# Kernel optimization log

Hardware: AMD Instinct MI355X
Metric: run time of the kernel (lower is better)

Reference implementation:

```python
import jax, jax.numpy as jnp
import numpy as np

N_FLUID, N_BOX, K_MAX, KS, NCELL = 6000, 3000, 80, 4, 64
RADIUS = np.float32(0.5 * 1.5 * 6 * 0.025)  # filter_extent / 2 = 0.1125


def _ball_to_cube(p):
    """Volume-preserving ball->cube mapping (open3d ContinuousConv convention).
    p: [..., 3] coordinates in the unit ball; returns coords in [-1,1]^3."""
    eps = 1e-12
    x, y, z = p[..., 0], p[..., 1], p[..., 2]
    sq = x * x + y * y + z * z
    norm = jnp.sqrt(sq)
    rxy2 = x * x + y * y
    # sphere -> cylinder (volume preserving)
    polar = 1.25 * z * z > rxy2
    s_pol = jnp.sqrt(3.0 * norm / (norm + jnp.abs(z) + eps))
    s_eq = norm / jnp.sqrt(rxy2 + eps)
    xc = jnp.where(polar, s_pol * x, s_eq * x)
    yc = jnp.where(polar, s_pol * y, s_eq * y)
    zc = jnp.where(polar, jnp.sign(z) * norm, 1.5 * z * s_eq)
    zero = sq < 1e-12
    xc = jnp.where(zero, 0.0, xc)
    yc = jnp.where(zero, 0.0, yc)
    zc = jnp.where(zero, 0.0, zc)
    # cylinder -> cube (area-preserving disc -> square on xy)
    rxy = jnp.sqrt(xc * xc + yc * yc)
    FP = 4.0 / np.pi
    safe_x = jnp.where(jnp.abs(xc) < eps, eps, xc)
    safe_y = jnp.where(jnp.abs(yc) < eps, eps, yc)
    cond = jnp.abs(xc) >= jnp.abs(yc)
    u1 = jnp.sign(xc) * rxy
    v1 = u1 * FP * jnp.arctan(yc / safe_x)
    v2 = jnp.sign(yc) * rxy
    u2 = v2 * FP * jnp.arctan(xc / safe_y)
    u = jnp.where(cond, u1, u2)
    v = jnp.where(cond, v1, v2)
    small = rxy < eps
    u = jnp.where(small, 0.0, u)
    v = jnp.where(small, 0.0, v)
    return jnp.stack([u, v, zc], axis=-1)


def build_neighbors(pos_in, pos_out, ignore_self):
    """Fixed-radius neighbor search (capped at K_MAX) + window + trilinear
    interpolation cells/weights. Returns idx [No,K], cells [No,K,8] int32,
    coef [No,K,8] (trilinear weight * poly6 window * validity)."""
    d = pos_in[None, :, :] - pos_out[:, None, :]            # [No,Ni,3]
    d2 = jnp.sum(d * d, axis=-1)
    if ignore_self:
        ii = jnp.arange(pos_out.shape[0])
        d2 = jnp.where(ii[:, None] == ii[None, :], jnp.inf, d2)
    neg = jnp.where(d2 <= RADIUS * RADIUS, -d2, -jnp.inf)
    vals, idx = jax.lax.top_k(neg, K_MAX)                   # [No,K]
    valid = (vals > -jnp.inf).astype(pos_in.dtype)
    rel = (pos_in[idx] - pos_out[:, None, :]) / RADIUS      # [No,K,3] unit ball
    r2 = jnp.sum(rel * rel, axis=-1)
    win = jnp.clip((1.0 - r2) ** 3, 0.0, 1.0) * valid       # poly6 window
    g = jnp.clip((_ball_to_cube(rel) + 1.0) * 0.5 * (KS - 1), 0.0, KS - 1.0)
    i0 = jnp.clip(jnp.floor(g), 0, KS - 2).astype(jnp.int32)
    t = g - i0.astype(g.dtype)
    cells, tw = [], []
    for dx in (0, 1):
        for dy in (0, 1):
            for dz in (0, 1):
                w = ((t[..., 0] if dx else 1.0 - t[..., 0])
                     * (t[..., 1] if dy else 1.0 - t[..., 1])
                     * (t[..., 2] if dz else 1.0 - t[..., 2]))
                cell = ((i0[..., 2] + dz) * KS + (i0[..., 1] + dy)) * KS + (i0[..., 0] + dx)
                cells.append(cell)
                tw.append(w)
    cells = jnp.stack(cells, axis=-1)                       # [No,K,8]
    coef = jnp.stack(tw, axis=-1) * win[..., None]          # [No,K,8]
    return idx, cells, coef


def apply_cconv(feats_in, idx, cells, coef, W, b):
    """Continuous conv: scatter neighbor feats into 64 kernel cells per query,
    then contract with the filter. W: [64, F, O]."""
    N, K = idx.shape
    F = feats_in.shape[-1]
    nf = feats_in[idx]                                      # [N,K,F]
    S = jnp.zeros((N * NCELL, F), feats_in.dtype)
    row = (jnp.arange(N, dtype=jnp.int32) * NCELL)[:, None]
    for c in range(8):                                      # 8 trilinear corners
        flat = (row + cells[..., c]).reshape(-1)
        S = S.at[flat].add((coef[..., c:c + 1] * nf).reshape(-1, F))
    return jnp.einsum('ncf,cfo->no', S.reshape(N, NCELL, F), W) + b


def setup_inputs() -> dict:
    key = jax.random.key(0)
    ks = jax.random.split(key, 16)

    def p(i, shape, scale=0.05):
        return (scale * jax.random.normal(ks[i], shape)).astype(jnp.float32)

    return {
        'pos': jax.random.uniform(ks[0], (N_FLUID, 3), dtype=jnp.float32),
        'vel': jax.random.normal(ks[1], (N_FLUID, 3), dtype=jnp.float32),
        'box': jax.random.uniform(ks[2], (N_BOX, 3), dtype=jnp.float32),
        'box_feats': jax.random.normal(ks[3], (N_BOX, 3), dtype=jnp.float32),
        'cf_w': p(4, (NCELL, 4, 32)), 'cf_b': jnp.zeros((32,), jnp.float32),
        'co_w': p(5, (NCELL, 3, 32)), 'co_b': jnp.zeros((32,), jnp.float32),
        'd0_w': p(6, (4, 32)), 'd0_b': jnp.zeros((32,), jnp.float32),
        'c1_w': p(7, (NCELL, 96, 64)), 'c1_b': jnp.zeros((64,), jnp.float32),
        'd1_w': p(8, (96, 64)), 'd1_b': jnp.zeros((64,), jnp.float32),
        'c2_w': p(9, (NCELL, 64, 64)), 'c2_b': jnp.zeros((64,), jnp.float32),
        'd2_w': p(10, (64, 64)), 'd2_b': jnp.zeros((64,), jnp.float32),
        'c3_w': p(11, (NCELL, 64, 3)), 'c3_b': jnp.zeros((3,), jnp.float32),
        'd3_w': p(12, (64, 3)), 'd3_b': jnp.zeros((3,), jnp.float32),
    }


def reference(pos, vel, box, box_feats, cf_w, cf_b, co_w, co_b, d0_w, d0_b,
              c1_w, c1_b, d1_w, d1_b, c2_w, c2_b, d2_w, d2_b, c3_w, c3_b,
              d3_w, d3_b):
    fidx, fcells, fcoef = build_neighbors(pos, pos, True)
    oidx, ocells, ocoef = build_neighbors(box, pos, False)
    ff = jnp.concatenate([jnp.ones_like(pos[:, :1]), vel], axis=-1)  # [N,4]
    a_cf = apply_cconv(ff, fidx, fcells, fcoef, cf_w, cf_b)
    a_co = apply_cconv(box_feats, oidx, ocells, ocoef, co_w, co_b)
    a_d0 = ff @ d0_w + d0_b
    x = jnp.concatenate([a_co, a_cf, a_d0], axis=-1)                 # [N,96]
    for cw, cb, dw, db in ((c1_w, c1_b, d1_w, d1_b),
                           (c2_w, c2_b, d2_w, d2_b),
                           (c3_w, c3_b, d3_w, d3_b)):
        h = jax.nn.relu(x)
        y = apply_cconv(h, fidx, fcells, fcoef, cw, cb) + (h @ dw + db)
        x = y + x if y.shape[-1] == x.shape[-1] else y
    return x * (1.0 / 128.0)  # pos_correction [N,3]
```

## Files before the change

### kernel.cpp

```cpp
#include <hip/hip_runtime.h>
#include <math.h>

namespace {

constexpr int NQ  = 6000;
constexpr int NB  = 3000;
constexpr int K   = 80;
constexpr float RAD = 0.1125f;
constexpr float R2  = RAD * RAD;
constexpr float EPSF = 1e-12f;

constexpr int GS  = 8;
constexpr int NC  = GS*GS*GS;
constexpr int NO  = 65 * 64;
constexpr int NBLK = (NQ + 3) / 4;
constexpr int NBLK8 = ((NBLK + 7) / 8) * 8;

typedef __attribute__((ext_vector_type(8))) short bf16x8;
typedef __attribute__((ext_vector_type(4))) float f32x4;

__device__ __forceinline__ float sgn(float x) {
    return (x > 0.f) ? 1.f : ((x < 0.f) ? -1.f : 0.f);
}

__device__ __forceinline__ unsigned int bf16rne(float f) {
    unsigned int u = __float_as_uint(f);
    return (u + 0x7fffu + ((u >> 16) & 1u)) >> 16;
}
__device__ __forceinline__ float bf16f(unsigned short u) {
    return __uint_as_float(((unsigned int)u) << 16);
}
__device__ __forceinline__ int cell_of(float x, float y, float z) {
    int cx = min(max((int)(x * (float)GS), 0), GS-1);
    int cy = min(max((int)(y * (float)GS), 0), GS-1);
    int cz = min(max((int)(z * (float)GS), 0), GS-1);
    return (cz*GS + cy)*GS + cx;
}

__device__ void coef_store(float ddx, float ddy, float ddz, int slot,
                           int* __restrict__ cells, float* __restrict__ coefs)
{
    float rx = ddx / RAD, ry = ddy / RAD, rz = ddz / RAD;
    float r2 = rx*rx + ry*ry + rz*rz;
    float w1 = 1.f - r2;
    float win = (w1 > 0.f) ? w1*w1*w1 : 0.f;
    float norm = sqrtf(r2);
    float rxy2 = rx*rx + ry*ry;
    float xc, yc, zc;
    if (r2 < 1e-12f) {
        xc = yc = zc = 0.f;
    } else if (1.25f * rz * rz > rxy2) {
        float s = sqrtf(3.0f * norm / (norm + fabsf(rz) + EPSF));
        xc = s * rx; yc = s * ry; zc = sgn(rz) * norm;
    } else {
        float s = norm / sqrtf(rxy2 + EPSF);
        xc = s * rx; yc = s * ry; zc = 1.5f * rz * s;
    }
    float rxy = sqrtf(xc*xc + yc*yc);
    const float FP = (float)(4.0 / M_PI);
    float u, v;
    if (rxy < EPSF) {
        u = 0.f; v = 0.f;
    } else if (fabsf(xc) >= fabsf(yc)) {
        float sx = (fabsf(xc) < EPSF) ? EPSF : xc;
        u = sgn(xc) * rxy;
        v = u * FP * atanf(yc / sx);
    } else {
        float sy = (fabsf(yc) < EPSF) ? EPSF : yc;
        v = sgn(yc) * rxy;
        u = v * FP * atanf(xc / sy);
    }
    float gx = fminf(fmaxf((u  + 1.f) * 0.5f * 3.f, 0.f), 3.f);
    float gy = fminf(fmaxf((v  + 1.f) * 0.5f * 3.f, 0.f), 3.f);
    float gz = fminf(fmaxf((zc + 1.f) * 0.5f * 3.f, 0.f), 3.f);
    int ix = min((int)floorf(gx), 2);
    int iy = min((int)floorf(gy), 2);
    int iz = min((int)floorf(gz), 2);
    float tx = gx - (float)ix, ty = gy - (float)iy, tz = gz - (float)iz;
    cells[slot] = iz*16 + iy*4 + ix;
    float wx[2] = {1.f - tx, tx}, wy[2] = {1.f - ty, ty}, wz[2] = {1.f - tz, tz};
    float* cf = coefs + (size_t)slot * 8;
#pragma unroll
    for (int c = 0; c < 8; ++c)
        cf[c] = wx[c >> 2] * wy[(c >> 1) & 1] * wz[c & 1] * win;
}

__global__ __launch_bounds__(512) void scan_kernel(
    const int* __restrict__ gcnt,
    int* __restrict__ gs_f, int* __restrict__ gs_b,
    int* __restrict__ cur_f, int* __restrict__ cur_b)
{
    __shared__ int tmp[NC];
    int tid = threadIdx.x;
#pragma unroll
    for (int a = 0; a < 2; ++a) {
        int cntv = gcnt[a*NC + tid];
        tmp[tid] = cntv;
        __syncthreads();
        for (int off = 1; off < NC; off <<= 1) {
            int v = (tid >= off) ? tmp[tid - off] : 0;
            __syncthreads();
            tmp[tid] += v;
            __syncthreads();
        }
        int* gsd = a ? gs_b : gs_f;
        int* cur = a ? cur_b : cur_f;
        int excl = tmp[tid] - cntv;
        gsd[tid] = excl;
        cur[tid] = excl;
        if (tid == NC - 1) gsd[NC] = tmp[tid];
        __syncthreads();
    }
}

__global__ __launch_bounds__(256) void scatter_pts_kernel(
    const float* __restrict__ pos, const float* __restrict__ box,
    int* __restrict__ cur_f, int* __restrict__ cur_b,
    float* __restrict__ spf, int* __restrict__ sif,
    float* __restrict__ spb, int* __restrict__ sib)
{
    int t = blockIdx.x * blockDim.x + threadIdx.x;
    if (t < NQ) {
        float x = pos[t*3], y = pos[t*3+1], z = pos[t*3+2];
        int dst = atomicAdd(&cur_f[cell_of(x,y,z)], 1);
        spf[dst*3] = x; spf[dst*3+1] = y; spf[dst*3+2] = z;
        sif[dst] = t;
    } else if (t < NQ + NB) {
        int b = t - NQ;
        float x = box[b*3], y = box[b*3+1], z = box[b*3+2];
        int dst = atomicAdd(&cur_b[cell_of(x,y,z)], 1);
        spb[dst*3] = x; spb[dst*3+1] = y; spb[dst*3+2] = z;
        sib[dst] = b;
    }
}

__global__ __launch_bounds__(256) void nn2gc_kernel(
    const float* __restrict__ pos,
    const float* __restrict__ spf, const int* __restrict__ sif, const int* __restrict__ gsf,
    const float* __restrict__ spb, const int* __restrict__ sib, const int* __restrict__ gsb,
    int* __restrict__ f_cnt, int* __restrict__ f_idx, float* __restrict__ f_d2,
    int* __restrict__ f_cell, float* __restrict__ f_coef,
    int* __restrict__ b_cnt, int* __restrict__ b_idx, float* __restrict__ b_d2,
    int* __restrict__ b_cell, float* __restrict__ b_coef)
{
    int gw = (blockIdx.x * blockDim.x + threadIdx.x) >> 6;
    int lane = threadIdx.x & 63;
    if (gw >= 2 * NQ) return;
    bool isF = gw < NQ;
    int wid = isF ? gw : gw - NQ;
    const float* sp = isF ? spf : spb;
    const int*   si = isF ? sif : sib;
    const int*   gs = isF ? gsf : gsb;
    int*   cnt   = isF ? f_cnt  : b_cnt;
    int*   idxs  = isF ? f_idx  : b_idx;
    float* d2s   = isF ? f_d2   : b_d2;
    int*   cells = isF ? f_cell : b_cell;
    float* coefs = isF ? f_coef : b_coef;
    float qx = pos[wid*3+0], qy = pos[wid*3+1], qz = pos[wid*3+2];
    int cx = min(max((int)(qx * (float)GS), 0), GS-1);
    int cy = min(max((int)(qy * (float)GS), 0), GS-1);
    int cz = min(max((int)(qz * (float)GS), 0), GS-1);
    int x0 = max(cx-1, 0), x1 = min(cx+1, GS-1);
    int base = wid * K;
    int c = 0;
    for (int dz = -1; dz <= 1; ++dz) {
        int z = cz + dz; if ((unsigned)z >= (unsigned)GS) continue;
        for (int dy = -1; dy <= 1; ++dy) {
            int y = cy + dy; if ((unsigned)y >= (unsigned)GS) continue;
            int row = (z*GS + y)*GS;
            int s0 = gs[row + x0], s1 = gs[row + x1 + 1];
            for (int j0 = s0; j0 < s1; j0 += 64) {
                int ii = j0 + lane;
                float d2 = 1e30f; int oj = 0;
                float ddx = 0.f, ddy = 0.f, ddz = 0.f;
                if (ii < s1) {
                    oj = si[ii];
                    ddx = sp[ii*3+0]-qx; ddy = sp[ii*3+1]-qy; ddz = sp[ii*3+2]-qz;
                    d2 = ddx*ddx + ddy*ddy + ddz*ddz;
                    if (isF && oj == wid) d2 = 1e30f;
                }
                bool hit = d2 <= R2;
                unsigned long long m = __ballot(hit);
                int pc = __popcll(m);
                if (pc == 0) continue;
                if (c + pc <= K) {
                    if (hit) {
                        int p = c + __popcll(m & ((1ull << lane) - 1ull));
                        idxs[base + p] = oj;
                        d2s [base + p] = d2;
                        coef_store(ddx, ddy, ddz, base + p, cells, coefs);
                    }
                    c += pc;
                } else {
                    while (m) {
                        int l = __ffsll((unsigned long long)m) - 1;
                        m &= m - 1ull;
                        float dd = __shfl(d2, l);
                        int jv = __shfl(oj, l);
                        float ax = __shfl(ddx, l), ay = __shfl(ddy, l), az = __shfl(ddz, l);
                        int slot = -1;
                        if (c < K) { slot = c; c++; }
                        else {
                            float mx = -1.f; int am = 0;
                            for (int s = 0; s < K; ++s) {
                                float v = d2s[base + s];
                                if (v > mx) { mx = v; am = s; }
                            }
                            if (dd < mx) slot = am;
                        }
                        if (slot >= 0 && lane == 0) {
                            idxs[base + slot] = jv;
                            d2s [base + slot] = dd;
                            coef_store(ax, ay, az, base + slot, cells, coefs);
                        }
                    }
                }
            }
        }
    }
    if (lane == 0) cnt[wid] = c;
}

template<int F>
__device__ void scatter_small_dev(
    const float* __restrict__ feats,
    const int* __restrict__ cnt, const int* __restrict__ nidx,
    const int* __restrict__ ncell, const float* __restrict__ ncoef,
    float* __restrict__ Sg, int blk)
{
    __shared__ __align__(16) float S4[4][64 * F];
    int tid = threadIdx.x, lane = tid & 63, w = tid >> 6;
    int n = blk * 4 + w;
    if (n >= NQ) return;
    float* Sw = S4[w];
    for (int i = lane; i < 64 * F; i += 64) Sw[i] = 0.f;
    int cn = cnt[n];
    int kk2 = 64 + lane;
    int cb1 = (lane < cn) ? ncell[n*K + lane] : 0;
    int j1  = (lane < cn) ? nidx [n*K + lane] : 0;
    int cb2 = (kk2 < cn) ? ncell[n*K + kk2] : 0;
    int j2  = (kk2 < cn) ? nidx [n*K + kk2] : 0;
    int c = lane & 7, f = lane >> 3;
    bool fok = f < F;
    const float* coefG = ncoef + (size_t)n * K * 8;

    float wgt = 0.f, v = 0.f; int cb = 0;
    if (cn > 0) {
        int j = __shfl(j1, 0); cb = __shfl(cb1, 0);
        if (fok) { wgt = coefG[c]; v = feats[(size_t)j * F + f]; }
    }
    for (int kk = 0; kk < cn; ++kk) {
        float wn = 0.f, vn = 0.f; int cbn = 0;
        int k1n = kk + 1;
        if (k1n < cn) {
            int jn = (k1n < 64) ? __shfl(j1, k1n) : __shfl(j2, k1n - 64);
            cbn    = (k1n < 64) ? __shfl(cb1, k1n) : __shfl(cb2, k1n - 64);
            if (fok) { wn = coefG[k1n*8 + c]; vn = feats[(size_t)jn * F + f]; }
        }
        if (fok) {
            int cell = cb + (c & 1)*16 + ((c >> 1) & 1)*4 + (c >> 2);
            Sw[cell*F + f] += wgt * v;
        }
        wgt = wn; v = vn; cb = cbn;
    }
    float* row = Sg + (size_t)n * (64 * F);
    for (int i = lane; i < 16 * F; i += 64)
        ((float4*)row)[i] = ((const float4*)Sw)[i];
}

__global__ __launch_bounds__(256) void scatter0_kernel(
    const float* __restrict__ ff,
    const int* __restrict__ f_cnt, const int* __restrict__ f_idx,
    const int* __restrict__ f_cell, const float* __restrict__ f_coef,
    const float* __restrict__ bfeat,
    const int* __restrict__ b_cnt, const int* __restrict__ b_idx,
    const int* __restrict__ b_cell, const float* __restrict__ b_coef,
    float* __restrict__ S_cf, float* __restrict__ S_co)
{
    constexpr int FB = (NQ + 3) / 4;
    if (blockIdx.x < FB)
        scatter_small_dev<4>(ff, f_cnt, f_idx, f_cell, f_coef, S_cf, blockIdx.x);
    else
        scatter_small_dev<3>(bfeat, b_cnt, b_idx, b_cell, b_coef, S_co, blockIdx.x - FB);
}

__global__ __launch_bounds__(256) void gemm0_kernel(
    const float* __restrict__ S_co, const float* __restrict__ S_cf,
    const float* __restrict__ coW, const float* __restrict__ cfW,
    const float* __restrict__ cob, const float* __restrict__ cfb,
    float* __restrict__ x1, int M)
{
    constexpr int O = 32, TX = 8, MT = 128, ASTR = 132;
    __shared__ float As[16][ASTR];
    __shared__ float Bs[16 * O];
    int which = blockIdx.y;
    const float* A    = which ? S_cf : S_co;
    const float* B    = which ? cfW  : coW;
    const float* bias = which ? cfb  : cob;
    int Kdim = which ? 256 : 192;
    int ooff = which ? 32 : 0;
    int tid = threadIdx.x;
    int tx = tid % TX, ty = tid / TX;
    int m0 = blockIdx.x * MT;
    int ntiles = Kdim >> 4;
    float acc[4][4] = {};
    for (int t = 0; t < ntiles; ++t) {
        int k0 = t << 4;
        __syncthreads();
#pragma unroll
        for (int l = 0; l < 2; ++l) {
            int idx = tid + l * 256;
            int mm = idx >> 2, k4 = idx & 3;
            int gm = m0 + mm; if (gm >= M) gm = M - 1;
            float4 av = *reinterpret_cast<const float4*>(A + (size_t)gm * Kdim + k0 + k4 * 4);
            As[k4*4+0][mm] = av.x; As[k4*4+1][mm] = av.y;
            As[k4*4+2][mm] = av.z; As[k4*4+3][mm] = av.w;
        }
        if (tid < 128)
            *reinterpret_cast<float4*>(&Bs[tid*4]) =
                *reinterpret_cast<const float4*>(B + (size_t)k0 * O + tid * 4);
        __syncthreads();
#pragma unroll
        for (int kk = 0; kk < 16; ++kk) {
            float4 av = *reinterpret_cast<const float4*>(&As[kk][ty*4]);
            float4 bv = *reinterpret_cast<const float4*>(&Bs[kk*O + tx*4]);
            float aa[4] = {av.x, av.y, av.z, av.w};
            float bb[4] = {bv.x, bv.y, bv.z, bv.w};
#pragma unroll
            for (int i = 0; i < 4; ++i)
#pragma unroll
                for (int jj = 0; jj < 4; ++jj)
                    acc[i][jj] += aa[i] * bb[jj];
        }
    }
#pragma unroll
    for (int i = 0; i < 4; ++i) {
        int gm = m0 + ty*4 + i;
        if (gm < M)
#pragma unroll
            for (int jj = 0; jj < 4; ++jj)
                x1[(size_t)gm * 96 + ooff + tx*4 + jj] = acc[i][jj] + bias[tx*4 + jj];
    }
}

template<int F>
__global__ __launch_bounds__(256) void gemmGm_kernel(
    const float* __restrict__ feats,
    const unsigned short* __restrict__ Bt,
    unsigned short* __restrict__ G,
    int M)
{
    constexpr int AST = F + 8;
    __shared__ unsigned short As[64 * AST];
    __shared__ unsigned short Bs[64 * AST];
    int tid = threadIdx.x, lane = tid & 63, wv = tid >> 6;
    int m0 = blockIdx.x * 64, no0 = blockIdx.y * 64;
    for (int i = tid; i < 64 * F / 4; i += 256) {
        int m = i / (F / 4), k4 = i % (F / 4);
        int gm = m0 + m; if (gm >= M) gm = M - 1;
        float4 av = *reinterpret_cast<const float4*>(feats + (size_t)gm * F + k4 * 4);
        uint2 o;
        o.x = bf16rne(fmaxf(av.x, 0.f)) | (bf16rne(fmaxf(av.y, 0.f)) << 16);
        o.y = bf16rne(fmaxf(av.z, 0.f)) | (bf16rne(fmaxf(av.w, 0.f)) << 16);
        *reinterpret_cast<uint2*>(As + m * AST + k4 * 4) = o;
    }
    for (int i = tid; i < 64 * F / 8; i += 256) {
        int n = i / (F / 8), k8 = i % (F / 8);
        *reinterpret_cast<uint4*>(Bs + n * AST + k8 * 8) =
            *reinterpret_cast<const uint4*>(Bt + (size_t)(no0 + n) * F + k8 * 8);
    }
    __syncthreads();
    int mr = lane & 15, quad = lane >> 4;
    f32x4 acc[4] = {{0.f,0.f,0.f,0.f},{0.f,0.f,0.f,0.f},
                    {0.f,0.f,0.f,0.f},{0.f,0.f,0.f,0.f}};
#pragma unroll
    for (int kc = 0; kc < F; kc += 32) {
        bf16x8 a = *reinterpret_cast<const bf16x8*>(As + (wv*16 + mr) * AST + kc + quad*8);
#pragma unroll
        for (int t = 0; t < 4; ++t) {
            bf16x8 b = *reinterpret_cast<const bf16x8*>(Bs + (t*16 + mr) * AST + kc + quad*8);
            acc[t] = __builtin_amdgcn_mfma_f32_16x16x32_bf16(a, b, acc[t], 0, 0, 0);
        }
    }
#pragma unroll
    for (int t = 0; t < 4; ++t) {
#pragma unroll
        for (int r = 0; r < 4; ++r) {
            int gm = m0 + wv*16 + quad*4 + r;
            if (gm < M)
                G[(size_t)gm * NO + no0 + t*16 + mr] = (unsigned short)bf16rne(acc[t][r]);
        }
    }
}

template<int FUSEY>
__global__ __launch_bounds__(256) void gatherG_kernel(
    const int* __restrict__ order,
    const int* __restrict__ cnt, const int* __restrict__ nidx,
    const int* __restrict__ ncell, const float* __restrict__ ncoef,
    const unsigned short* __restrict__ G,
    const float* __restrict__ cb, const float* __restrict__ db,
    const float* __restrict__ resid, float* __restrict__ out,
    const float* __restrict__ W3p, float* __restrict__ Y)
{
    __shared__ __align__(16) float coefL[K * 8];
    __shared__ int jL[K];
    __shared__ int cbL[K];
    __shared__ float part[3][64];
    __shared__ float xs[64];
    int lb = (blockIdx.x & 7) * (gridDim.x >> 3) + (blockIdx.x >> 3);
    int tid = threadIdx.x;
    int wv = tid >> 6, lane = tid & 63;
    int n = order[lb];
    int cn = cnt[n];
    {
        const float4* src = (const float4*)(ncoef + (size_t)n * K * 8);
        float4* dst = (float4*)coefL;
        for (int i = tid; i < cn * 2; i += 256) dst[i] = src[i];
        for (int i = tid; i < cn; i += 256) {
            jL[i]  = nidx [n*K + i];
            cbL[i] = ncell[n*K + i];
        }
    }
    __syncthreads();
    float a0 = 0.f, a1 = 0.f, a2 = 0.f, a3 = 0.f;
#pragma unroll 2
    for (int k = wv; k < cn; k += 4) {
        int j    = jL[k];
        int cbse = cbL[k];
        float4 cA = *reinterpret_cast<const float4*>(coefL + k*8);
        float4 cB = *reinterpret_cast<const float4*>(coefL + k*8 + 4);
        const unsigned short* Gj = G + (size_t)j * NO + (size_t)cbse * 64 + lane;
        a0 += cA.x * bf16f(Gj[ 0 * 64]);
        a1 += cA.y * bf16f(Gj[16 * 64]);
        a2 += cA.z * bf16f(Gj[ 4 * 64]);
        a3 += cA.w * bf16f(Gj[20 * 64]);
        a0 += cB.x * bf16f(Gj[ 1 * 64]);
        a1 += cB.y * bf16f(Gj[17 * 64]);
        a2 += cB.z * bf16f(Gj[ 5 * 64]);
        a3 += cB.w * bf16f(Gj[21 * 64]);
    }
    float s = (a0 + a1) + (a2 + a3);
    if (wv > 0) part[wv - 1][lane] = s;
    __syncthreads();
    if (wv == 0) {
        float acc = cb[lane] + db[lane] + s
                  + part[0][lane] + part[1][lane] + part[2][lane];
        acc += bf16f(G[(size_t)n * NO + 64*64 + lane]);
        if (resid) acc += resid[(size_t)n * 64 + lane];
        if (!FUSEY) {
            out[(size_t)n * 64 + lane] = acc;
        } else {
            xs[lane] = fmaxf(acc, 0.f);
        }
    }
    if (FUSEY) {
        __syncthreads();
        for (int t = tid; t < 195; t += 256) {
            float sum = 0.f;
#pragma unroll 16
            for (int f = 0; f < 64; ++f) sum += xs[f] * W3p[f*195 + t];
            Y[(size_t)n * 195 + t] = sum;
        }
    }
}

__global__ __launch_bounds__(256) void prep_kernel(
    const float* __restrict__ c1w, const float* __restrict__ d1w,
    const float* __restrict__ c2w, const float* __restrict__ d2w,
    const float* __restrict__ c3w, const float* __restrict__ d3w,
    const float* __restrict__ pos, const float* __restrict__ box,
    const float* __restrict__ vel,
    const float* __restrict__ d0w, const float* __restrict__ d0b,
    unsigned short* __restrict__ Bt1, unsigned short* __restrict__ Bt2,
    float* __restrict__ W3p, float* __restrict__ ff, float* __restrict__ x1,
    int* __restrict__ gcnt)
{
    int stride = gridDim.x * blockDim.x;
    int gid = blockIdx.x * blockDim.x + threadIdx.x;
    for (int i = gid; i < NQ + NB; i += stride) {
        const float* p = (i < NQ) ? pos + (size_t)i*3 : box + (size_t)(i-NQ)*3;
        atomicAdd(&gcnt[((i < NQ) ? 0 : NC) + cell_of(p[0], p[1], p[2])], 1);
    }
    for (int i = gid; i < NO * 96; i += stride) {
        int n = i / 96, f = i % 96, c = n >> 6, o = n & 63;
        float v = (c < 64) ? c1w[((size_t)c*96 + f)*64 + o] : d1w[f*64 + o];
        Bt1[i] = (unsigned short)bf16rne(v);
    }
    for (int i = gid; i < NO * 64; i += stride) {
        int n = i / 64, f = i % 64, c = n >> 6, o = n & 63;
        float v = (c < 64) ? c2w[((size_t)c*64 + f)*64 + o] : d2w[f*64 + o];
        Bt2[i] = (unsigned short)bf16rne(v);
    }
    for (int i = gid; i < 64 * 195; i += stride) {
        int f = i / 195, r = i % 195, c = r / 3, o = r % 3;
        W3p[i] = (c < 64) ? c3w[(c*64 + f)*3 + o] : d3w[f*3 + o];
    }
    for (int i = gid; i < NQ; i += stride) {
        ff[i*4+0] = 1.f;
        ff[i*4+1] = vel[i*3+0];
        ff[i*4+2] = vel[i*3+1];
        ff[i*4+3] = vel[i*3+2];
    }
    for (int i = gid; i < NQ * 32; i += stride) {
        int n = i >> 5, o = i & 31;
        float acc = d0b[o] + d0w[o]
                  + vel[n*3+0] * d0w[32 + o]
                  + vel[n*3+1] * d0w[64 + o]
                  + vel[n*3+2] * d0w[96 + o];
        x1[n*96 + 64 + o] = acc;
    }
}

__global__ __launch_bounds__(256) void gather3_kernel(
    const int* __restrict__ order,
    const int* __restrict__ cnt, const int* __restrict__ nidx,
    const int* __restrict__ ncell, const float* __restrict__ ncoef,
    const float* __restrict__ Y,
    const float* __restrict__ cb3, const float* __restrict__ db3,
    float* __restrict__ out)
{
    int lb = (blockIdx.x & 7) * (gridDim.x >> 3) + (blockIdx.x >> 3);
    int gw = lb * 4 + ((int)threadIdx.x >> 6);
    int lane = threadIdx.x & 63;
    if (gw >= NQ) return;
    int n = order[gw];
    int cn = cnt[n];
    float a0 = 0.f, a1 = 0.f, a2 = 0.f;
#pragma unroll
    for (int seg = 0; seg < 2; ++seg) {
        int kidx = seg * 64 + lane;
        if (kidx < cn) {
            int j  = nidx [n*K + kidx];
            int cb = ncell[n*K + kidx];
            const float* cf = ncoef + (size_t)(n*K + kidx) * 8;
            const float* Yj = Y + (size_t)j * 195;
#pragma unroll
            for (int c = 0; c < 8; ++c) {
                int cell = cb + (c & 1)*16 + ((c >> 1) & 1)*4 + (c >> 2);
                float wgt = cf[c];
                const float* Tp = Yj + cell*3;
                a0 += wgt * Tp[0];
                a1 += wgt * Tp[1];
                a2 += wgt * Tp[2];
            }
        }
    }
#pragma unroll
    for (int s = 32; s > 0; s >>= 1) {
        a0 += __shfl_down(a0, s);
        a1 += __shfl_down(a1, s);
        a2 += __shfl_down(a2, s);
    }
    if (lane == 0) {
        const float* Yn = Y + (size_t)n * 195 + 192;
        out[n*3+0] = (a0 + Yn[0] + cb3[0] + db3[0]) * (1.f/128.f);
        out[n*3+1] = (a1 + Yn[1] + cb3[1] + db3[1]) * (1.f/128.f);
        out[n*3+2] = (a2 + Yn[2] + cb3[2] + db3[2]) * (1.f/128.f);
    }
}

}

extern "C" void kernel_launch(void* const* d_in, const int* in_sizes, int n_in,
                              void* d_out, int out_size, void* d_ws, size_t ws_size,
                              hipStream_t stream)
{
    const float* pos       = (const float*)d_in[0];
    const float* vel       = (const float*)d_in[1];
    const float* box       = (const float*)d_in[2];
    const float* box_feats = (const float*)d_in[3];
    const float* cf_w = (const float*)d_in[4];  const float* cf_b = (const float*)d_in[5];
    const float* co_w = (const float*)d_in[6];  const float* co_b = (const float*)d_in[7];
    const float* d0_w = (const float*)d_in[8];  const float* d0_b = (const float*)d_in[9];
    const float* c1_w = (const float*)d_in[10]; const float* c1_b = (const float*)d_in[11];
    const float* d1_w = (const float*)d_in[12]; const float* d1_b = (const float*)d_in[13];
    const float* c2_w = (const float*)d_in[14]; const float* c2_b = (const float*)d_in[15];
    const float* d2_w = (const float*)d_in[16]; const float* d2_b = (const float*)d_in[17];
    const float* c3_w = (const float*)d_in[18]; const float* c3_b = (const float*)d_in[19];
    const float* d3_w = (const float*)d_in[20]; const float* d3_b = (const float*)d_in[21];

    char* wsb = (char*)d_ws;
    size_t off = 0;
    auto alloc = [&](size_t bytes) {
        void* p = wsb + off;
        off = (off + bytes + 255) & ~(size_t)255;
        return p;
    };
    char*  Graw = (char*)alloc((size_t)NQ * NO * 2 + 4096);
    unsigned short* G = (unsigned short*)Graw;
    float* f_d2 = (float*)Graw;
    float* b_d2 = (float*)Graw + (size_t)NQ * K;
    float* S_cf = (float*)Graw;
    float* S_co = (float*)Graw + (size_t)NQ * 256;
    int*   f_cnt  = (int*)  alloc((size_t)NQ * 4);
    int*   f_idx  = (int*)  alloc((size_t)NQ * K * 4);
    int*   f_cell = (int*)  alloc((size_t)NQ * K * 4);
    float* f_coef = (float*)alloc((size_t)NQ * K * 8 * 4);
    int*   b_cnt  = (int*)  alloc((size_t)NQ * 4);
    int*   b_idx  = (int*)  alloc((size_t)NQ * K * 4);
    int*   b_cell = (int*)  alloc((size_t)NQ * K * 4);
    float* b_coef = (float*)alloc((size_t)NQ * K * 8 * 4);
    float* ff     = (float*)alloc((size_t)NQ * 4 * 4);
    float* x1     = (float*)alloc((size_t)NQ * 96 * 4);
    float* x2     = (float*)alloc((size_t)NQ * 64 * 4);
    unsigned short* Bt1 = (unsigned short*)alloc((size_t)NO * 96 * 2);
    unsigned short* Bt2 = (unsigned short*)alloc((size_t)NO * 64 * 2);
    float* W3p    = (float*)alloc((size_t)64 * 195 * 4);
    float* Y      = (float*)alloc((size_t)NQ * 195 * 4);
    int*   gcnt   = (int*)  alloc((size_t)2 * NC * 4);
    int*   gs_f   = (int*)  alloc((size_t)(NC + 1) * 4);
    int*   gs_b   = (int*)  alloc((size_t)(NC + 1) * 4);
    int*   cur_f  = (int*)  alloc((size_t)NC * 4);
    int*   cur_b  = (int*)  alloc((size_t)NC * 4);
    float* spf    = (float*)alloc((size_t)NQ * 3 * 4);
    int*   sif    = (int*)  alloc((size_t)NQ * 4);
    float* spb    = (float*)alloc((size_t)NB * 3 * 4);
    int*   sib    = (int*)  alloc((size_t)NB * 4);

    dim3 b256(256);
    hipMemsetAsync(gcnt, 0, (size_t)2 * NC * 4, stream);
    prep_kernel<<<512, b256, 0, stream>>>(c1_w, d1_w, c2_w, d2_w, c3_w, d3_w,
                                          pos, box, vel, d0_w, d0_b,
                                          Bt1, Bt2, W3p, ff, x1, gcnt);
    scan_kernel<<<1, 512, 0, stream>>>(gcnt, gs_f, gs_b, cur_f, cur_b);
    scatter_pts_kernel<<<(NQ + NB + 255)/256, b256, 0, stream>>>(
        pos, box, cur_f, cur_b, spf, sif, spb, sib);
    nn2gc_kernel<<<(2*NQ*64 + 255)/256, b256, 0, stream>>>(
        pos, spf, sif, gs_f, spb, sib, gs_b,
        f_cnt, f_idx, f_d2, f_cell, f_coef,
        b_cnt, b_idx, b_d2, b_cell, b_coef);
    scatter0_kernel<<<2*((NQ+3)/4), b256, 0, stream>>>(
        ff, f_cnt, f_idx, f_cell, f_coef,
        box_feats, b_cnt, b_idx, b_cell, b_coef, S_cf, S_co);
    gemm0_kernel<<<dim3((NQ+127)/128, 2), b256, 0, stream>>>(
        S_co, S_cf, co_w, cf_w, co_b, cf_b, x1, NQ);
    gemmGm_kernel<96><<<dim3((NQ+63)/64, NO/64), b256, 0, stream>>>(x1, Bt1, G, NQ);
    gatherG_kernel<0><<<NQ, b256, 0, stream>>>(sif, f_cnt, f_idx, f_cell, f_coef,
        G, c1_b, d1_b, nullptr, x2, nullptr, nullptr);
    gemmGm_kernel<64><<<dim3((NQ+63)/64, NO/64), b256, 0, stream>>>(x2, Bt2, G, NQ);
    gatherG_kernel<1><<<NQ, b256, 0, stream>>>(sif, f_cnt, f_idx, f_cell, f_coef,
        G, c2_b, d2_b, x2, nullptr, W3p, Y);
    gather3_kernel<<<NBLK8, b256, 0, stream>>>(sif, f_cnt, f_idx, f_cell, f_coef,
        Y, c3_b, d3_b, (float*)d_out);

    (void)in_sizes; (void)n_in; (void)out_size; (void)ws_size;
    (void)f_d2; (void)b_d2;
}
```

Before: 281.9 us.

## Precompute per-point cell projections for first conv layer and gather instead of scatter+GEMM

Replaces the first-layer scatter into per-point cell buffers followed by an FP32 GEMM with a precomputed per-source-point table (features times per-cell weights, stored as bf16) built in the prep kernel. A new gather kernel then sums trilinear-weighted table entries over neighbours. This drops the scatter-to-LDS pass and the separate gemm0 launch, at the cost of writing two large bf16 tables in prep and reduced precision. Separately, the MFMA G-GEMM now loops over 5 output tiles per block, keeping the A tile resident and shrinking the grid y-dimension from 65 to 13.

Measured after the change: 270.0 us. -4.2%, faster.

```diff
diff --git a/kernel.cpp b/kernel.cpp
--- a/kernel.cpp
+++ b/kernel.cpp
@@ -221,125 +221,82 @@
     if (lane == 0) cnt[wid] = c;
 }
 
-template<int F>
-__device__ void scatter_small_dev(
-    const float* __restrict__ feats,
-    const int* __restrict__ cnt, const int* __restrict__ nidx,
-    const int* __restrict__ ncell, const float* __restrict__ ncoef,
-    float* __restrict__ Sg, int blk)
-{
-    __shared__ __align__(16) float S4[4][64 * F];
-    int tid = threadIdx.x, lane = tid & 63, w = tid >> 6;
-    int n = blk * 4 + w;
-    if (n >= NQ) return;
-    float* Sw = S4[w];
-    for (int i = lane; i < 64 * F; i += 64) Sw[i] = 0.f;
-    int cn = cnt[n];
-    int kk2 = 64 + lane;
-    int cb1 = (lane < cn) ? ncell[n*K + lane] : 0;
-    int j1  = (lane < cn) ? nidx [n*K + lane] : 0;
-    int cb2 = (kk2 < cn) ? ncell[n*K + kk2] : 0;
-    int j2  = (kk2 < cn) ? nidx [n*K + kk2] : 0;
-    int c = lane & 7, f = lane >> 3;
-    bool fok = f < F;
-    const float* coefG = ncoef + (size_t)n * K * 8;
-
-    float wgt = 0.f, v = 0.f; int cb = 0;
-    if (cn > 0) {
-        int j = __shfl(j1, 0); cb = __shfl(cb1, 0);
-        if (fok) { wgt = coefG[c]; v = feats[(size_t)j * F + f]; }
-    }
-    for (int kk = 0; kk < cn; ++kk) {
-        float wn = 0.f, vn = 0.f; int cbn = 0;
-        int k1n = kk + 1;
-        if (k1n < cn) {
-            int jn = (k1n < 64) ? __shfl(j1, k1n) : __shfl(j2, k1n - 64);
-            cbn    = (k1n < 64) ? __shfl(cb1, k1n) : __shfl(cb2, k1n - 64);
-            if (fok) { wn = coefG[k1n*8 + c]; vn = feats[(size_t)jn * F + f]; }
-        }
-        if (fok) {
-            int cell = cb + (c & 1)*16 + ((c >> 1) & 1)*4 + (c >> 2);
-            Sw[cell*F + f] += wgt * v;
-        }
-        wgt = wn; v = vn; cb = cbn;
-    }
-    float* row = Sg + (size_t)n * (64 * F);
-    for (int i = lane; i < 16 * F; i += 64)
-        ((float4*)row)[i] = ((const float4*)Sw)[i];
-}
-
-__global__ __launch_bounds__(256) void scatter0_kernel(
-    const float* __restrict__ ff,
+__global__ __launch_bounds__(256) void gather0_kernel(
+    const int* __restrict__ order,
     const int* __restrict__ f_cnt, const int* __restrict__ f_idx,
     const int* __restrict__ f_cell, const float* __restrict__ f_coef,
-    const float* __restrict__ bfeat,
     const int* __restrict__ b_cnt, const int* __restrict__ b_idx,
     const int* __restrict__ b_cell, const float* __restrict__ b_coef,
-    float* __restrict__ S_cf, float* __restrict__ S_co)
-{
-    constexpr int FB = (NQ + 3) / 4;
-    if (blockIdx.x < FB)
-        scatter_small_dev<4>(ff, f_cnt, f_idx, f_cell, f_coef, S_cf, blockIdx.x);
-    else
-        scatter_small_dev<3>(bfeat, b_cnt, b_idx, b_cell, b_coef, S_co, blockIdx.x - FB);
-}
-
-__global__ __launch_bounds__(256) void gemm0_kernel(
-    const float* __restrict__ S_co, const float* __restrict__ S_cf,
-    const float* __restrict__ coW, const float* __restrict__ cfW,
-    const float* __restrict__ cob, const float* __restrict__ cfb,
-    float* __restrict__ x1, int M)
-{
-    constexpr int O = 32, TX = 8, MT = 128, ASTR = 132;
-    __shared__ float As[16][ASTR];
-    __shared__ float Bs[16 * O];
-    int which = blockIdx.y;
-    const float* A    = which ? S_cf : S_co;
-    const float* B    = which ? cfW  : coW;
-    const float* bias = which ? cfb  : cob;
-    int Kdim = which ? 256 : 192;
-    int ooff = which ? 32 : 0;
+    const unsigned short* __restrict__ G0f, const unsigned short* __restrict__ G0b,
+    const float* __restrict__ cfb, const float* __restrict__ cob,
+    float* __restrict__ x1)
+{
+    __shared__ __align__(16) float coefF[K * 8];
+    __shared__ __align__(16) float coefB[K * 8];
+    __shared__ int jF[K], cF[K], jB[K], cBx[K];
+    __shared__ float partF[8][32], partB[8][32];
+    int lb = (blockIdx.x & 7) * (gridDim.x >> 3) + (blockIdx.x >> 3);
     int tid = threadIdx.x;
-    int tx = tid % TX, ty = tid / TX;
-    int m0 = blockIdx.x * MT;
-    int ntiles = Kdim >> 4;
-    float acc[4][4] = {};
-    for (int t = 0; t < ntiles; ++t) {
-        int k0 = t << 4;
-        __syncthreads();
-#pragma unroll
-        for (int l = 0; l < 2; ++l) {
-            int idx = tid + l * 256;
-            int mm = idx >> 2, k4 = idx & 3;
-            int gm = m0 + mm; if (gm >= M) gm = M - 1;
-            float4 av = *reinterpret_cast<const float4*>(A + (size_t)gm * Kdim + k0 + k4 * 4);
-            As[k4*4+0][mm] = av.x; As[k4*4+1][mm] = av.y;
-            As[k4*4+2][mm] = av.z; As[k4*4+3][mm] = av.w;
-        }
-        if (tid < 128)
-            *reinterpret_cast<float4*>(&Bs[tid*4]) =
-                *reinterpret_cast<const float4*>(B + (size_t)k0 * O + tid * 4);
-        __syncthreads();
-#pragma unroll
-        for (int kk = 0; kk < 16; ++kk) {
-            float4 av = *reinterpret_cast<const float4*>(&As[kk][ty*4]);
-            float4 bv = *reinterpret_cast<const float4*>(&Bs[kk*O + tx*4]);
-            float aa[4] = {av.x, av.y, av.z, av.w};
-            float bb[4] = {bv.x, bv.y, bv.z, bv.w};
-#pragma unroll
-            for (int i = 0; i < 4; ++i)
-#pragma unroll
-                for (int jj = 0; jj < 4; ++jj)
-                    acc[i][jj] += aa[i] * bb[jj];
-        }
-    }
-#pragma unroll
-    for (int i = 0; i < 4; ++i) {
-        int gm = m0 + ty*4 + i;
-        if (gm < M)
-#pragma unroll
-            for (int jj = 0; jj < 4; ++jj)
-                x1[(size_t)gm * 96 + ooff + tx*4 + jj] = acc[i][jj] + bias[tx*4 + jj];
+    int wv = tid >> 6, lane = tid & 63;
+    int h = lane >> 5, o = lane & 31;
+    int r = wv * 2 + h;
+    int n = order[lb];
+    int cnf = f_cnt[n], cnb = b_cnt[n];
+    {
+        const float4* srcF = (const float4*)(f_coef + (size_t)n * K * 8);
+        const float4* srcB = (const float4*)(b_coef + (size_t)n * K * 8);
+        for (int i = tid; i < cnf * 2; i += 256) ((float4*)coefF)[i] = srcF[i];
+        for (int i = tid; i < cnb * 2; i += 256) ((float4*)coefB)[i] = srcB[i];
+        for (int i = tid; i < cnf; i += 256) { jF[i] = f_idx[n*K + i]; cF[i]  = f_cell[n*K + i]; }
+        for (int i = tid; i < cnb; i += 256) { jB[i] = b_idx[n*K + i]; cBx[i] = b_cell[n*K + i]; }
+    }
+    __syncthreads();
+    float af = 0.f;
+#pragma unroll 2
+    for (int k = r; k < cnf; k += 8) {
+        const unsigned short* Gj = G0f + (size_t)jF[k] * 2048 + (size_t)cF[k] * 32 + o;
+        float4 cA = *reinterpret_cast<const float4*>(coefF + k*8);
+        float4 cB = *reinterpret_cast<const float4*>(coefF + k*8 + 4);
+        af += cA.x * bf16f(Gj[ 0 * 32]);
+        af += cA.y * bf16f(Gj[16 * 32]);
+        af += cA.z * bf16f(Gj[ 4 * 32]);
+        af += cA.w * bf16f(Gj[20 * 32]);
+        af += cB.x * bf16f(Gj[ 1 * 32]);
+        af += cB.y * bf16f(Gj[17 * 32]);
+        af += cB.z * bf16f(Gj[ 5 * 32]);
+        af += cB.w * bf16f(Gj[21 * 32]);
+    }
+    float ab = 0.f;
+#pragma unroll 2
+    for (int k = r; k < cnb; k += 8) {
+        const unsigned short* Gj = G0b + (size_t)jB[k] * 2048 + (size_t)cBx[k] * 32 + o;
+        float4 cA = *reinterpret_cast<const float4*>(coefB + k*8);
+        float4 cB = *reinterpret_cast<const float4*>(coefB + k*8 + 4);
+        ab += cA.x * bf16f(Gj[ 0 * 32]);
+        ab += cA.y * bf16f(Gj[16 * 32]);
+        ab += cA.z * bf16f(Gj[ 4 * 32]);
+        ab += cA.w * bf16f(Gj[20 * 32]);
+        ab += cB.x * bf16f(Gj[ 1 * 32]);
+        ab += cB.y * bf16f(Gj[17 * 32]);
+        ab += cB.z * bf16f(Gj[ 5 * 32]);
+        ab += cB.w * bf16f(Gj[21 * 32]);
+    }
+    partF[r][o] = af;
+    partB[r][o] = ab;
+    __syncthreads();
+    if (tid < 64) {
+        int oo = tid & 31;
+        if (tid < 32) {
+            float s = cfb[oo];
+#pragma unroll
+            for (int q = 0; q < 8; ++q) s += partF[q][oo];
+            x1[(size_t)n * 96 + 32 + oo] = s;
+        } else {
+            float s = cob[oo];
+#pragma unroll
+            for (int q = 0; q < 8; ++q) s += partB[q][oo];
+            x1[(size_t)n * 96 + oo] = s;
+        }
     }
 }
 
@@ -350,45 +307,51 @@
     unsigned short* __restrict__ G,
     int M)
 {
+    constexpr int NT = 5;
     constexpr int AST = F + 8;
     __shared__ unsigned short As[64 * AST];
     __shared__ unsigned short Bs[64 * AST];
     int tid = threadIdx.x, lane = tid & 63, wv = tid >> 6;
-    int m0 = blockIdx.x * 64, no0 = blockIdx.y * 64;
+    int m0 = blockIdx.x * 64;
+    int nt0 = blockIdx.y * NT;
     for (int i = tid; i < 64 * F / 4; i += 256) {
         int m = i / (F / 4), k4 = i % (F / 4);
         int gm = m0 + m; if (gm >= M) gm = M - 1;
         float4 av = *reinterpret_cast<const float4*>(feats + (size_t)gm * F + k4 * 4);
-        uint2 o;
-        o.x = bf16rne(fmaxf(av.x, 0.f)) | (bf16rne(fmaxf(av.y, 0.f)) << 16);
-        o.y = bf16rne(fmaxf(av.z, 0.f)) | (bf16rne(fmaxf(av.w, 0.f)) << 16);
-        *reinterpret_cast<uint2*>(As + m * AST + k4 * 4) = o;
-    }
-    for (int i = tid; i < 64 * F / 8; i += 256) {
-        int n = i / (F / 8), k8 = i % (F / 8);
-        *reinterpret_cast<uint4*>(Bs + n * AST + k8 * 8) =
-            *reinterpret_cast<const uint4*>(Bt + (size_t)(no0 + n) * F + k8 * 8);
-    }
-    __syncthreads();
+        uint2 ov;
+        ov.x = bf16rne(fmaxf(av.x, 0.f)) | (bf16rne(fmaxf(av.y, 0.f)) << 16);
+        ov.y = bf16rne(fmaxf(av.z, 0.f)) | (bf16rne(fmaxf(av.w, 0.f)) << 16);
+        *reinterpret_cast<uint2*>(As + m * AST + k4 * 4) = ov;
+    }
     int mr = lane & 15, quad = lane >> 4;
-    f32x4 acc[4] = {{0.f,0.f,0.f,0.f},{0.f,0.f,0.f,0.f},
-                    {0.f,0.f,0.f,0.f},{0.f,0.f,0.f,0.f}};
-#pragma unroll
-    for (int kc = 0; kc < F; kc += 32) {
-        bf16x8 a = *reinterpret_cast<const bf16x8*>(As + (wv*16 + mr) * AST + kc + quad*8);
-#pragma unroll
-        for (int t = 0; t < 4; ++t) {
-            bf16x8 b = *reinterpret_cast<const bf16x8*>(Bs + (t*16 + mr) * AST + kc + quad*8);
-            acc[t] = __builtin_amdgcn_mfma_f32_16x16x32_bf16(a, b, acc[t], 0, 0, 0);
-        }
-    }
-#pragma unroll
-    for (int t = 0; t < 4; ++t) {
-#pragma unroll
-        for (int r = 0; r < 4; ++r) {
-            int gm = m0 + wv*16 + quad*4 + r;
-            if (gm < M)
-                G[(size_t)gm * NO + no0 + t*16 + mr] = (unsigned short)bf16rne(acc[t][r]);
+    for (int t = 0; t < NT; ++t) {
+        int no0 = (nt0 + t) * 64;
+        __syncthreads();
+        for (int i = tid; i < 64 * F / 8; i += 256) {
+            int nn = i / (F / 8), k8 = i % (F / 8);
+            *reinterpret_cast<uint4*>(Bs + nn * AST + k8 * 8) =
+                *reinterpret_cast<const uint4*>(Bt + (size_t)(no0 + nn) * F + k8 * 8);
+        }
+        __syncthreads();
+        f32x4 acc[4] = {{0.f,0.f,0.f,0.f},{0.f,0.f,0.f,0.f},
+                        {0.f,0.f,0.f,0.f},{0.f,0.f,0.f,0.f}};
+#pragma unroll
+        for (int kc = 0; kc < F; kc += 32) {
+            bf16x8 a = *reinterpret_cast<const bf16x8*>(As + (wv*16 + mr) * AST + kc + quad*8);
+#pragma unroll
+            for (int q = 0; q < 4; ++q) {
+                bf16x8 b = *reinterpret_cast<const bf16x8*>(Bs + (q*16 + mr) * AST + kc + quad*8);
+                acc[q] = __builtin_amdgcn_mfma_f32_16x16x32_bf16(a, b, acc[q], 0, 0, 0);
+            }
+        }
+#pragma unroll
+        for (int q = 0; q < 4; ++q) {
+#pragma unroll
+            for (int rr = 0; rr < 4; ++rr) {
+                int gm = m0 + wv*16 + quad*4 + rr;
+                if (gm < M)
+                    G[(size_t)gm * NO + no0 + q*16 + mr] = (unsigned short)bf16rne(acc[q][rr]);
+            }
         }
     }
 }
@@ -470,10 +433,12 @@
     const float* __restrict__ c2w, const float* __restrict__ d2w,
     const float* __restrict__ c3w, const float* __restrict__ d3w,
     const float* __restrict__ pos, const float* __restrict__ box,
-    const float* __restrict__ vel,
+    const float* __restrict__ vel, const float* __restrict__ bfeat,
+    const float* __restrict__ cfw, const float* __restrict__ cow,
     const float* __restrict__ d0w, const float* __restrict__ d0b,
     unsigned short* __restrict__ Bt1, unsigned short* __restrict__ Bt2,
-    float* __restrict__ W3p, float* __restrict__ ff, float* __restrict__ x1,
+    unsigned short* __restrict__ G0f, unsigned short* __restrict__ G0b,
+    float* __restrict__ W3p, float* __restrict__ x1,
     int* __restrict__ gcnt)
 {
     int stride = gridDim.x * blockDim.x;
@@ -482,6 +447,24 @@
         const float* p = (i < NQ) ? pos + (size_t)i*3 : box + (size_t)(i-NQ)*3;
         atomicAdd(&gcnt[((i < NQ) ? 0 : NC) + cell_of(p[0], p[1], p[2])], 1);
     }
+    for (int i = gid; i < NQ * 1024; i += stride) {
+        int j = i >> 10, rr = i & 1023, c = rr >> 4, op = (rr & 15) * 2;
+        float vx = vel[j*3+0], vy = vel[j*3+1], vz = vel[j*3+2];
+        const float* w = cfw + (size_t)c * 128;
+        float s0 = w[op]   + vx*w[32+op]   + vy*w[64+op]   + vz*w[96+op];
+        float s1 = w[op+1] + vx*w[32+op+1] + vy*w[64+op+1] + vz*w[96+op+1];
+        *reinterpret_cast<unsigned int*>(G0f + (size_t)j * 2048 + c*32 + op) =
+            bf16rne(s0) | (bf16rne(s1) << 16);
+    }
+    for (int i = gid; i < NB * 1024; i += stride) {
+        int j = i >> 10, rr = i & 1023, c = rr >> 4, op = (rr & 15) * 2;
+        float b0 = bfeat[j*3+0], b1 = bfeat[j*3+1], b2 = bfeat[j*3+2];
+        const float* w = cow + (size_t)c * 96;
+        float s0 = b0*w[op]   + b1*w[32+op]   + b2*w[64+op];
+        float s1 = b0*w[op+1] + b1*w[32+op+1] + b2*w[64+op+1];
+        *reinterpret_cast<unsigned int*>(G0b + (size_t)j * 2048 + c*32 + op) =
+            bf16rne(s0) | (bf16rne(s1) << 16);
+    }
     for (int i = gid; i < NO * 96; i += stride) {
         int n = i / 96, f = i % 96, c = n >> 6, o = n & 63;
         float v = (c < 64) ? c1w[((size_t)c*96 + f)*64 + o] : d1w[f*64 + o];
@@ -495,12 +478,6 @@
     for (int i = gid; i < 64 * 195; i += stride) {
         int f = i / 195, r = i % 195, c = r / 3, o = r % 3;
         W3p[i] = (c < 64) ? c3w[(c*64 + f)*3 + o] : d3w[f*3 + o];
-    }
-    for (int i = gid; i < NQ; i += stride) {
-        ff[i*4+0] = 1.f;
-        ff[i*4+1] = vel[i*3+0];
-        ff[i*4+2] = vel[i*3+1];
-        ff[i*4+3] = vel[i*3+2];
     }
     for (int i = gid; i < NQ * 32; i += stride) {
         int n = i >> 5, o = i & 31;
@@ -591,8 +568,8 @@
     unsigned short* G = (unsigned short*)Graw;
     float* f_d2 = (float*)Graw;
     float* b_d2 = (float*)Graw + (size_t)NQ * K;
-    float* S_cf = (float*)Graw;
-    float* S_co = (float*)Graw + (size_t)NQ * 256;
+    unsigned short* G0f = (unsigned short*)(Graw + ((size_t)4 << 20));
+    unsigned short* G0b = (unsigned short*)(Graw + ((size_t)32 << 20));
     int*   f_cnt  = (int*)  alloc((size_t)NQ * 4);
     int*   f_idx  = (int*)  alloc((size_t)NQ * K * 4);
     int*   f_cell = (int*)  alloc((size_t)NQ * K * 4);
@@ -601,7 +578,6 @@
     int*   b_idx  = (int*)  alloc((size_t)NQ * K * 4);
     int*   b_cell = (int*)  alloc((size_t)NQ * K * 4);
     float* b_coef = (float*)alloc((size_t)NQ * K * 8 * 4);
-    float* ff     = (float*)alloc((size_t)NQ * 4 * 4);
     float* x1     = (float*)alloc((size_t)NQ * 96 * 4);
     float* x2     = (float*)alloc((size_t)NQ * 64 * 4);
     unsigned short* Bt1 = (unsigned short*)alloc((size_t)NO * 96 * 2);
@@ -621,8 +597,9 @@
     dim3 b256(256);
     hipMemsetAsync(gcnt, 0, (size_t)2 * NC * 4, stream);
     prep_kernel<<<512, b256, 0, stream>>>(c1_w, d1_w, c2_w, d2_w, c3_w, d3_w,
-                                          pos, box, vel, d0_w, d0_b,
-                                          Bt1, Bt2, W3p, ff, x1, gcnt);
+                                          pos, box, vel, box_feats, cf_w, co_w,
+                                          d0_w, d0_b,
+                                          Bt1, Bt2, G0f, G0b, W3p, x1, gcnt);
     scan_kernel<<<1, 512, 0, stream>>>(gcnt, gs_f, gs_b, cur_f, cur_b);
     scatter_pts_kernel<<<(NQ + NB + 255)/256, b256, 0, stream>>>(
         pos, box, cur_f, cur_b, spf, sif, spb, sib);
@@ -630,15 +607,14 @@
         pos, spf, sif, gs_f, spb, sib, gs_b,
         f_cnt, f_idx, f_d2, f_cell, f_coef,
         b_cnt, b_idx, b_d2, b_cell, b_coef);
-    scatter0_kernel<<<2*((NQ+3)/4), b256, 0, stream>>>(
-        ff, f_cnt, f_idx, f_cell, f_coef,
-        box_feats, b_cnt, b_idx, b_cell, b_coef, S_cf, S_co);
-    gemm0_kernel<<<dim3((NQ+127)/128, 2), b256, 0, stream>>>(
-        S_co, S_cf, co_w, cf_w, co_b, cf_b, x1, NQ);
-    gemmGm_kernel<96><<<dim3((NQ+63)/64, NO/64), b256, 0, stream>>>(x1, Bt1, G, NQ);
+    gather0_kernel<<<NQ, b256, 0, stream>>>(sif,
+        f_cnt, f_idx, f_cell, f_coef,
+        b_cnt, b_idx, b_cell, b_coef,
+        G0f, G0b, cf_b, co_b, x1);
+    gemmGm_kernel<96><<<dim3((NQ+63)/64, 13), b256, 0, stream>>>(x1, Bt1, G, NQ);
     gatherG_kernel<0><<<NQ, b256, 0, stream>>>(sif, f_cnt, f_idx, f_cell, f_coef,
         G, c1_b, d1_b, nullptr, x2, nullptr, nullptr);
-    gemmGm_kernel<64><<<dim3((NQ+63)/64, NO/64), b256, 0, stream>>>(x2, Bt2, G, NQ);
+    gemmGm_kernel<64><<<dim3((NQ+63)/64, 13), b256, 0, stream>>>(x2, Bt2, G, NQ);
     gatherG_kernel<1><<<NQ, b256, 0, stream>>>(sif, f_cnt, f_idx, f_cell, f_coef,
         G, c2_b, d2_b, x2, nullptr, W3p, Y);
     gather3_kernel<<<NBLK8, b256, 0, stream>>>(sif, f_cnt, f_idx, f_cell, f_coef,
```
